# Performance work log

Measured on AMD Instinct MI355X. Metric: run time of the kernel, lower is better.

The kernel has to match this reference:

```python
import jax, jax.numpy as jnp
import numpy as np

N, E = 50000, 600000
NODE_DIM, EDGE_DIM, MSG_DIM = 128, 64, 128


def setup_inputs() -> dict:
    key = jax.random.key(0)
    ks = jax.random.split(key, 8)
    s = 0.05
    return {
        "node_features": jax.random.normal(ks[0], (N, NODE_DIM), jnp.float32),
        "edge_features": jax.random.normal(ks[1], (E, EDGE_DIM), jnp.float32),
        "edge_index": jax.random.randint(ks[2], (2, E), 0, N, jnp.int32),
        "We1": jax.random.normal(ks[3], (2 * NODE_DIM + EDGE_DIM, 32), jnp.float32) * s,
        "be1": jnp.zeros((32,), jnp.float32),
        "We2": jax.random.normal(ks[4], (32, MSG_DIM), jnp.float32) * s,
        "be2": jnp.zeros((MSG_DIM,), jnp.float32),
        "Wn1": jax.random.normal(ks[5], (NODE_DIM + MSG_DIM, 64), jnp.float32) * s,
        "bn1": jnp.zeros((64,), jnp.float32),
        "Wn2": jax.random.normal(ks[6], (64, MSG_DIM), jnp.float32) * s,
        "bn2": jnp.zeros((MSG_DIM,), jnp.float32),
    }


def reference(node_features, edge_features, edge_index,
              We1, be1, We2, be2, Wn1, bn1, Wn2, bn2):
    src, dst = edge_index[0], edge_index[1]
    src_f = node_features[src]            # [E, node_dim] gather
    dst_f = node_features[dst]            # [E, node_dim] gather
    # edge message encoder: 2-layer MLP with ReLU
    edge_in = jnp.concatenate([src_f, dst_f, edge_features], axis=1)  # [E, 2*nd+ed]
    h = jax.nn.relu(edge_in @ We1 + be1)
    edge_msg = jax.nn.relu(h @ We2 + be2)  # [E, msg_dim]
    # node message encoder
    node_in = jnp.concatenate([dst_f, edge_msg], axis=1)  # [E, nd+md]
    h2 = jax.nn.relu(node_in @ Wn1 + bn1)
    node_msg = jax.nn.relu(h2 @ Wn2 + bn2)  # [E, msg_dim]
    # scatter-sum over destination nodes (replaces the O(N) python loop)
    agg = jax.ops.segment_sum(node_msg, dst, num_segments=node_features.shape[0])
    return node_features + agg
```

## Files before the change

### kernel.cpp

```cpp
#include <hip/hip_runtime.h>
#include <hip/hip_bf16.h>

constexpr int N_NODES = 50000;
constexpr int N_EDGES = 600000;
constexpr int ND = 128;
constexpr int ED = 64;
constexpr int MD = 128;
constexpr int H1 = 32;
constexpr int H2 = 64;

typedef __attribute__((ext_vector_type(8))) short short8;
typedef __attribute__((ext_vector_type(4))) float f32x4;
typedef __attribute__((ext_vector_type(4))) unsigned int uint32x4;

#define MFMA16(a, b, c) __builtin_amdgcn_mfma_f32_16x16x32_bf16((a), (b), (c), 0, 0, 0)

constexpr int COUNTS_PAD = 53248;
constexpr size_t WS_MSGS    = 0;
constexpr size_t WS_PRE     = WS_MSGS + (size_t)N_EDGES * MD * 2;
constexpr size_t WS_POS     = WS_PRE + (size_t)N_NODES * 128 * 2;
constexpr size_t WS_COUNTS  = WS_POS + (size_t)N_EDGES * 4;
constexpr size_t WS_OFFSETS = WS_COUNTS + (size_t)COUNTS_PAD * 4;
constexpr size_t WS_WFE     = ((WS_OFFSETS + (size_t)(N_NODES + 1) * 4 + 15) / 16) * 16;
constexpr size_t WS_WFN     = WS_WFE + (size_t)44 * 64 * 16;
constexpr size_t WS_END     = WS_WFN + (size_t)32 * 64 * 16;

__device__ inline float bflo(unsigned u) { return __uint_as_float(u << 16); }
__device__ inline float bfhi(unsigned u) { return __uint_as_float(u & 0xffff0000u); }
__device__ inline short f2bf(float f) {
    __hip_bfloat16 h = __float2bfloat16(f);
    return *reinterpret_cast<short*>(&h);
}
__device__ inline unsigned pkbf(float a, float b) {
    unsigned r;
    asm("v_cvt_pk_bf16_f32 %0, %1, %2" : "=v"(r) : "v"(a), "v"(b));
    return r;
}
__device__ inline unsigned prelu(float a, float b) {
    return pkbf(fmaxf(a, 0.0f), fmaxf(b, 0.0f));
}
__device__ inline short8 pack8(unsigned w0, unsigned w1, unsigned w2, unsigned w3) {
    uint32x4 t{w0, w1, w2, w3};
    return __builtin_bit_cast(short8, t);
}

__device__ inline int hperm(int kt, int kq) {
    return (kt * 2 + ((kq >> 2) & 1)) * 16 + ((kq >> 3) & 3) * 4 + (kq & 3);
}

__global__ __launch_bounds__(256) void wprep(
    const float* __restrict__ We1, const float* __restrict__ We2,
    const float* __restrict__ Wn1, const float* __restrict__ Wn2,
    short8* __restrict__ wfE, short8* __restrict__ wfN)
{
    const int g = blockIdx.x * 256 + threadIdx.x;
    const int lane = g & 63;
    const int f = g >> 6;
    const int m16 = lane & 15, quad = lane >> 4;
    short v[8];
    if (f < 44) {
        #pragma unroll
        for (int j = 0; j < 8; ++j) {
            const int kq = quad * 8 + j;
            float s;
            if (f < 4) {
                const int kt = f >> 1, mt = f & 1;
                s = We1[(size_t)(2 * ND + kt * 32 + kq) * H1 + mt * 16 + m16];
            } else if (f < 12) {
                const int mt = f - 4;
                s = We2[(size_t)hperm(0, kq) * MD + mt * 16 + m16];
            } else if (f < 28) {
                const int ff = f - 12, kt = ff >> 2, mt = ff & 3;
                s = Wn1[(size_t)(ND + hperm(kt, kq)) * H2 + mt * 16 + m16];
            } else {
                const int ff = f - 28, kt = ff >> 3, mt = ff & 7;
                s = Wn2[(size_t)hperm(kt, kq) * MD + mt * 16 + m16];
            }
            v[j] = f2bf(s);
        }
        wfE[g] = short8{v[0], v[1], v[2], v[3], v[4], v[5], v[6], v[7]};
    } else {
        const int ff = f - 44, kt = ff >> 3, nt = ff & 7;
        const int n = nt * 16 + m16;
        #pragma unroll
        for (int j = 0; j < 8; ++j) {
            const int k = kt * 32 + quad * 8 + j;
            float s;
            if (n < 32)      s = We1[(size_t)k * H1 + n];
            else if (n < 64) s = We1[(size_t)(ND + k) * H1 + (n - 32)];
            else             s = Wn1[(size_t)k * H2 + (n - 64)];
            v[j] = f2bf(s);
        }
        wfN[(size_t)(f - 44) * 64 + lane] = short8{v[0], v[1], v[2], v[3], v[4], v[5], v[6], v[7]};
    }
}

__global__ __launch_bounds__(256) void hist_pos(const int* __restrict__ eidx,
                                                int* __restrict__ counts,
                                                int* __restrict__ pos) {
    const int e = blockIdx.x * 256 + threadIdx.x;
    if (e < N_EDGES) pos[e] = atomicAdd(&counts[eidx[N_EDGES + e]], 1);
}

__global__ __launch_bounds__(1024) void scan_kernel(const int* __restrict__ counts,
                                                    int* __restrict__ offsets) {
    constexpr int T = 1024;
    const int tid = threadIdx.x;
    const int base = tid * 52;
    int4 v[13];
    int s = 0;
    const int4* pc = (const int4*)(counts + base);
    #pragma unroll
    for (int i = 0; i < 13; ++i) {
        v[i] = pc[i];
        s += v[i].x + v[i].y + v[i].z + v[i].w;
    }
    __shared__ int sm[T];
    sm[tid] = s;
    __syncthreads();
    for (int off = 1; off < T; off <<= 1) {
        const int t = (tid >= off) ? sm[tid - off] : 0;
        __syncthreads();
        sm[tid] += t;
        __syncthreads();
    }
    int run = sm[tid] - s;
    #pragma unroll
    for (int i = 0; i < 13; ++i) {
        const int idx = base + i * 4;
        if (idx     <= N_NODES) offsets[idx]     = run;  run += v[i].x;
        if (idx + 1 <= N_NODES) offsets[idx + 1] = run;  run += v[i].y;
        if (idx + 2 <= N_NODES) offsets[idx + 2] = run;  run += v[i].z;
        if (idx + 3 <= N_NODES) offsets[idx + 3] = run;  run += v[i].w;
    }
}

__global__ __launch_bounds__(256) void node_pre_mfma(
    const float* __restrict__ nf, const short8* __restrict__ wfN,
    unsigned short* __restrict__ pre)
{
    __shared__ short ost[4][2048];
    const int tid = threadIdx.x;
    const int w = tid >> 6, lane = tid & 63;
    const int m16 = lane & 15, quad = lane >> 4;
    const int n0 = blockIdx.x * 64 + w * 16;

    short8 a[4];
    #pragma unroll
    for (int kt = 0; kt < 4; ++kt) {
        const int node = min(n0 + m16, N_NODES - 1);
        const float* pn = nf + (size_t)node * ND + kt * 32 + quad * 8;
        const float4 f0 = *(const float4*)pn;
        const float4 f1 = *(const float4*)(pn + 4);
        a[kt] = pack8(pkbf(f0.x, f0.y), pkbf(f0.z, f0.w),
                      pkbf(f1.x, f1.y), pkbf(f1.z, f1.w));
    }
    f32x4 acc[8];
    #pragma unroll
    for (int nt = 0; nt < 8; ++nt) acc[nt] = f32x4{0.f, 0.f, 0.f, 0.f};
    #pragma unroll
    for (int kt = 0; kt < 4; ++kt) {
        #pragma unroll
        for (int nt = 0; nt < 8; ++nt)
            acc[nt] = MFMA16(a[kt], wfN[(size_t)(kt * 8 + nt) * 64 + lane], acc[nt]);
    }
    short* o = &ost[w][0];
    #pragma unroll
    for (int nt = 0; nt < 8; ++nt)
        #pragma unroll
        for (int r = 0; r < 4; ++r)
            o[(quad * 4 + r) * 128 + nt * 16 + m16] = f2bf(acc[nt][r]);
    asm volatile("s_waitcnt lgkmcnt(0)" ::: "memory");
    #pragma unroll
    for (int i = 0; i < 4; ++i) {
        const int row = i * 4 + quad;
        const int node = n0 + row;
        if (node < N_NODES) {
            const uint4 v = ((const uint4*)(o + row * 128))[m16];
            *((uint4*)(pre + (size_t)node * 128) + m16) = v;
        }
    }
}

__global__ __launch_bounds__(256, 4) void edge_mfma(
    const float* __restrict__ ef, const int* __restrict__ eidx,
    const unsigned short* __restrict__ pre,
    const int* __restrict__ pos, const int* __restrict__ offsets,
    const short8* __restrict__ wfE,
    const float* __restrict__ be1, const float* __restrict__ be2,
    const float* __restrict__ bn1, const float* __restrict__ bn2,
    unsigned short* __restrict__ msgs)
{
    constexpr int TE = 128;
    __shared__ __align__(16) char sws[4][9216];
    __shared__ int slotlds[TE];

    const int tid = threadIdx.x;
    const int e0 = blockIdx.x * TE;
    const bool hasB = (e0 + 64) < N_EDGES;
    const int w = tid >> 6, lane = tid & 63;
    const int m16 = lane & 15, q = lane >> 4;
    const int er0 = w * 16;
    char* swsb = &sws[w][0];

    float4 efv[2][4];
    {
        const float* pe = ef + (size_t)(e0 + er0 + m16) * ED + q * 8;
        efv[0][0] = *(const float4*)pe;
        efv[0][1] = *(const float4*)(pe + 4);
        efv[0][2] = *(const float4*)(pe + 32);
        efv[0][3] = *(const float4*)(pe + 36);
        if (hasB) {
            const float* pe2 = pe + (size_t)64 * ED;
            efv[1][0] = *(const float4*)pe2;
            efv[1][1] = *(const float4*)(pe2 + 4);
            efv[1][2] = *(const float4*)(pe2 + 32);
            efv[1][3] = *(const float4*)(pe2 + 36);
        }
    }

    {
        const int et = tid >> 2, p4 = tid & 3;
        const int eA = e0 + et;
        const int srcA = eidx[eA];
        const int dstA = eidx[N_EDGES + eA];
        const uint4* paA = (const uint4*)(pre + (size_t)srcA * 128);
        const uint4* pdA = (const uint4*)(pre + (size_t)dstA * 128);
        const uint4 uaA = paA[p4];
        const uint4 udA = pdA[4 + p4];
        const uint4 s0A = pdA[8 + 2 * p4];
        const uint4 s1A = pdA[9 + 2 * p4];
        const int slA = offsets[dstA] + pos[eA];

        uint4 uaB, udB, s0B, s1B;
        int slB = 0;
        if (hasB) {
            const int eB = eA + 64;
            const int srcB = eidx[eB];
            const int dstB = eidx[N_EDGES + eB];
            const uint4* paB = (const uint4*)(pre + (size_t)srcB * 128);
            const uint4* pdB = (const uint4*)(pre + (size_t)dstB * 128);
            uaB = paB[p4];
            udB = pdB[4 + p4];
            s0B = pdB[8 + 2 * p4];
            s1B = pdB[9 + 2 * p4];
            slB = offsets[dstB] + pos[eB];
        }
        const float4 b0 = ((const float4*)be1)[2 * p4];
        const float4 b1 = ((const float4*)be1)[2 * p4 + 1];

        char* wbase = &sws[et >> 4][0] + (et & 15) * 144;
        {
            float4 r0, r1;
            r0.x = bflo(uaA.x) + bflo(udA.x) + b0.x;
            r0.y = bfhi(uaA.x) + bfhi(udA.x) + b0.y;
            r0.z = bflo(uaA.y) + bflo(udA.y) + b0.z;
            r0.w = bfhi(uaA.y) + bfhi(udA.y) + b0.w;
            r1.x = bflo(uaA.z) + bflo(udA.z) + b1.x;
            r1.y = bfhi(uaA.z) + bfhi(udA.z) + b1.y;
            r1.z = bflo(uaA.w) + bflo(udA.w) + b1.z;
            r1.w = bfhi(uaA.w) + bfhi(udA.w) + b1.w;
            *(float4*)(wbase + p4 * 32) = r0;
            *(float4*)(wbase + p4 * 32 + 16) = r1;
            *(uint4*)(wbase + 2304 + p4 * 32) = s0A;
            *(uint4*)(wbase + 2304 + p4 * 32 + 16) = s1A;
            if (p4 == 3) slotlds[et] = slA;
        }
        if (hasB) {
            float4 r0, r1;
            r0.x = bflo(uaB.x) + bflo(udB.x) + b0.x;
            r0.y = bfhi(uaB.x) + bfhi(udB.x) + b0.y;
            r0.z = bflo(uaB.y) + bflo(udB.y) + b0.z;
            r0.w = bfhi(uaB.y) + bfhi(udB.y) + b0.w;
            r1.x = bflo(uaB.z) + bflo(udB.z) + b1.x;
            r1.y = bfhi(uaB.z) + bfhi(udB.z) + b1.y;
            r1.z = bflo(uaB.w) + bflo(udB.w) + b1.z;
            r1.w = bfhi(uaB.w) + bfhi(udB.w) + b1.w;
            *(float4*)(wbase + 4608 + p4 * 32) = r0;
            *(float4*)(wbase + 4608 + p4 * 32 + 16) = r1;
            *(uint4*)(wbase + 4608 + 2304 + p4 * 32) = s0B;
            *(uint4*)(wbase + 4608 + 2304 + p4 * 32 + 16) = s1B;
            if (p4 == 3) slotlds[64 + et] = slB;
        }
    }
    asm volatile("s_waitcnt lgkmcnt(0)" ::: "memory");

    short8 aef[2][2];
    #pragma unroll
    for (int t = 0; t < 2; ++t) {
        aef[t][0] = pack8(pkbf(efv[t][0].x, efv[t][0].y), pkbf(efv[t][0].z, efv[t][0].w),
                          pkbf(efv[t][1].x, efv[t][1].y), pkbf(efv[t][1].z, efv[t][1].w));
        aef[t][1] = pack8(pkbf(efv[t][2].x, efv[t][2].y), pkbf(efv[t][2].z, efv[t][2].w),
                          pkbf(efv[t][3].x, efv[t][3].y), pkbf(efv[t][3].z, efv[t][3].w));
    }

    f32x4 acc1[2][2];
    #pragma unroll
    for (int t = 0; t < 2; ++t)
        #pragma unroll
        for (int mt = 0; mt < 2; ++mt)
            acc1[t][mt] = *(const f32x4*)(swsb + t * 4608 + m16 * 144 + mt * 64 + q * 16);
    #pragma unroll
    for (int kt = 0; kt < 2; ++kt)
        #pragma unroll
        for (int mt = 0; mt < 2; ++mt) {
            const short8 wf = wfE[(size_t)(kt * 2 + mt) * 64 + lane];
            acc1[0][mt] = MFMA16(wf, aef[0][kt], acc1[0][mt]);
            acc1[1][mt] = MFMA16(wf, aef[1][kt], acc1[1][mt]);
        }

    short8 b2[2];
    #pragma unroll
    for (int t = 0; t < 2; ++t)
        b2[t] = pack8(prelu(acc1[t][0][0], acc1[t][0][1]), prelu(acc1[t][0][2], acc1[t][0][3]),
                      prelu(acc1[t][1][0], acc1[t][1][1]), prelu(acc1[t][1][2], acc1[t][1][3]));

    f32x4 acc2[2][8];
    #pragma unroll
    for (int mt = 0; mt < 8; ++mt) {
        const float4 bb = *(const float4*)(be2 + mt * 16 + q * 4);
        const short8 wf = wfE[(size_t)(4 + mt) * 64 + lane];
        acc2[0][mt] = f32x4{bb.x, bb.y, bb.z, bb.w};
        acc2[1][mt] = acc2[0][mt];
        acc2[0][mt] = MFMA16(wf, b2[0], acc2[0][mt]);
        acc2[1][mt] = MFMA16(wf, b2[1], acc2[1][mt]);
    }
    short8 b3[2][4];
    #pragma unroll
    for (int t = 0; t < 2; ++t)
        #pragma unroll
        for (int kt = 0; kt < 4; ++kt)
            b3[t][kt] = pack8(prelu(acc2[t][2 * kt][0], acc2[t][2 * kt][1]),
                              prelu(acc2[t][2 * kt][2], acc2[t][2 * kt][3]),
                              prelu(acc2[t][2 * kt + 1][0], acc2[t][2 * kt + 1][1]),
                              prelu(acc2[t][2 * kt + 1][2], acc2[t][2 * kt + 1][3]));

    f32x4 acc3[2][4];
    #pragma unroll
    for (int mt = 0; mt < 4; ++mt) {
        const float4 bb = *(const float4*)(bn1 + mt * 16 + q * 4);
        #pragma unroll
        for (int t = 0; t < 2; ++t) {
            const uint2 ua = *(const uint2*)(swsb + t * 4608 + 2304 + m16 * 144 + mt * 32 + q * 8);
            acc3[t][mt] = f32x4{bb.x + bflo(ua.x), bb.y + bfhi(ua.x),
                                bb.z + bflo(ua.y), bb.w + bfhi(ua.y)};
        }
    }
    #pragma unroll
    for (int kt = 0; kt < 4; ++kt)
        #pragma unroll
        for (int mt = 0; mt < 4; ++mt) {
            const short8 wf = wfE[(size_t)(12 + kt * 4 + mt) * 64 + lane];
            acc3[0][mt] = MFMA16(wf, b3[0][kt], acc3[0][mt]);
            acc3[1][mt] = MFMA16(wf, b3[1][kt], acc3[1][mt]);
        }
    short8 b4[2][2];
    #pragma unroll
    for (int t = 0; t < 2; ++t)
        #pragma unroll
        for (int kt = 0; kt < 2; ++kt)
            b4[t][kt] = pack8(prelu(acc3[t][2 * kt][0], acc3[t][2 * kt][1]),
                              prelu(acc3[t][2 * kt][2], acc3[t][2 * kt][3]),
                              prelu(acc3[t][2 * kt + 1][0], acc3[t][2 * kt + 1][1]),
                              prelu(acc3[t][2 * kt + 1][2], acc3[t][2 * kt + 1][3]));

    f32x4 acc4[2][8];
    #pragma unroll
    for (int mt = 0; mt < 8; ++mt) {
        const float4 bb = *(const float4*)(bn2 + mt * 16 + q * 4);
        acc4[0][mt] = f32x4{bb.x, bb.y, bb.z, bb.w};
        acc4[1][mt] = acc4[0][mt];
    }
    #pragma unroll
    for (int kt = 0; kt < 2; ++kt)
        #pragma unroll
        for (int mt = 0; mt < 8; ++mt) {
            const short8 wf = wfE[(size_t)(28 + kt * 8 + mt) * 64 + lane];
            acc4[0][mt] = MFMA16(wf, b4[0][kt], acc4[0][mt]);
            acc4[1][mt] = MFMA16(wf, b4[1][kt], acc4[1][mt]);
        }

    #pragma unroll
    for (int t = 0; t < 2; ++t)
        #pragma unroll
        for (int mt = 0; mt < 8; ++mt) {
            uint2 wv;
            wv.x = prelu(acc4[t][mt][0], acc4[t][mt][1]);
            wv.y = prelu(acc4[t][mt][2], acc4[t][mt][3]);
            *(uint2*)(swsb + t * 4608 + m16 * 272 + mt * 32 + q * 8) = wv;
        }
    asm volatile("s_waitcnt lgkmcnt(0)" ::: "memory");

    #pragma unroll
    for (int i = 0; i < 4; ++i) {
        const int row = i * 4 + q;
        const int slA = slotlds[er0 + row];
        const uint4 vA = *(const uint4*)(swsb + row * 272 + m16 * 16);
        *((uint4*)(msgs + (size_t)slA * 128) + m16) = vA;
    }
    if (hasB) {
        #pragma unroll
        for (int i = 0; i < 4; ++i) {
            const int row = i * 4 + q;
            const int slB = slotlds[64 + er0 + row];
            const uint4 vB = *(const uint4*)(swsb + 4608 + row * 272 + m16 * 16);
            *((uint4*)(msgs + (size_t)slB * 128) + m16) = vB;
        }
    }
}

__global__ __launch_bounds__(256) void gather2(
    const float* __restrict__ nf,
    const uint4* __restrict__ msgs4,
    const int* __restrict__ offsets,
    float* __restrict__ out)
{
    const int node = blockIdx.x * 16 + (threadIdx.x >> 4);
    const int m16 = threadIdx.x & 15;

    const float4* pn = (const float4*)(nf + (size_t)node * ND) + m16 * 2;
    const float4 n0 = pn[0];
    const float4 n1 = pn[1];

    const int beg = offsets[node];
    const int end = offsets[node + 1];

    float4 sA0{0.f, 0.f, 0.f, 0.f}, sA1{0.f, 0.f, 0.f, 0.f};
    float4 sB0{0.f, 0.f, 0.f, 0.f}, sB1{0.f, 0.f, 0.f, 0.f};
    const uint4* p = msgs4 + (size_t)beg * 16 + m16;
    int i = beg;
    for (; i + 3 < end; i += 4, p += 64) {
        const uint4 u0 = p[0];
        const uint4 u1 = p[16];
        const uint4 u2 = p[32];
        const uint4 u3 = p[48];
        sA0.x += bflo(u0.x); sA0.y += bfhi(u0.x); sA0.z += bflo(u0.y); sA0.w += bfhi(u0.y);
        sA1.x += bflo(u0.z); sA1.y += bfhi(u0.z); sA1.z += bflo(u0.w); sA1.w += bfhi(u0.w);
        sB0.x += bflo(u1.x); sB0.y += bfhi(u1.x); sB0.z += bflo(u1.y); sB0.w += bfhi(u1.y);
        sB1.x += bflo(u1.z); sB1.y += bfhi(u1.z); sB1.z += bflo(u1.w); sB1.w += bfhi(u1.w);
        sA0.x += bflo(u2.x); sA0.y += bfhi(u2.x); sA0.z += bflo(u2.y); sA0.w += bfhi(u2.y);
        sA1.x += bflo(u2.z); sA1.y += bfhi(u2.z); sA1.z += bflo(u2.w); sA1.w += bfhi(u2.w);
        sB0.x += bflo(u3.x); sB0.y += bfhi(u3.x); sB0.z += bflo(u3.y); sB0.w += bfhi(u3.y);
        sB1.x += bflo(u3.z); sB1.y += bfhi(u3.z); sB1.z += bflo(u3.w); sB1.w += bfhi(u3.w);
    }
    for (; i < end; ++i, p += 16) {
        const uint4 u = p[0];
        sA0.x += bflo(u.x); sA0.y += bfhi(u.x); sA0.z += bflo(u.y); sA0.w += bfhi(u.y);
        sA1.x += bflo(u.z); sA1.y += bfhi(u.z); sA1.z += bflo(u.w); sA1.w += bfhi(u.w);
    }
    float4 s0, s1;
    s0.x = sA0.x + sB0.x + n0.x; s0.y = sA0.y + sB0.y + n0.y;
    s0.z = sA0.z + sB0.z + n0.z; s0.w = sA0.w + sB0.w + n0.w;
    s1.x = sA1.x + sB1.x + n1.x; s1.y = sA1.y + sB1.y + n1.y;
    s1.z = sA1.z + sB1.z + n1.z; s1.w = sA1.w + sB1.w + n1.w;

    float4* po = (float4*)(out + (size_t)node * ND) + m16 * 2;
    po[0] = s0;
    po[1] = s1;
}

extern "C" void kernel_launch(void* const* d_in, const int* in_sizes, int n_in,
                              void* d_out, int out_size, void* d_ws, size_t ws_size,
                              hipStream_t stream) {
    const float* nf  = (const float*)d_in[0];
    const float* ef  = (const float*)d_in[1];
    const int*  eidx = (const int*)d_in[2];
    const float* We1 = (const float*)d_in[3];
    const float* be1 = (const float*)d_in[4];
    const float* We2 = (const float*)d_in[5];
    const float* be2 = (const float*)d_in[6];
    const float* Wn1 = (const float*)d_in[7];
    const float* bn1 = (const float*)d_in[8];
    const float* Wn2 = (const float*)d_in[9];
    const float* bn2 = (const float*)d_in[10];
    float* out = (float*)d_out;

    char* ws = (char*)d_ws;
    unsigned short* msgs = (unsigned short*)(ws + WS_MSGS);
    unsigned short* pre  = (unsigned short*)(ws + WS_PRE);
    int* pos             = (int*)(ws + WS_POS);
    int* counts          = (int*)(ws + WS_COUNTS);
    int* offsets         = (int*)(ws + WS_OFFSETS);
    short8* wfE          = (short8*)(ws + WS_WFE);
    short8* wfN          = (short8*)(ws + WS_WFN);
    (void)ws_size; (void)WS_END;

    hipMemsetAsync(counts, 0, (size_t)COUNTS_PAD * 4, stream);
    wprep<<<19, 256, 0, stream>>>(We1, We2, Wn1, Wn2, wfE, wfN);
    hist_pos<<<(N_EDGES + 255) / 256, 256, 0, stream>>>(eidx, counts, pos);
    scan_kernel<<<1, 1024, 0, stream>>>(counts, offsets);
    node_pre_mfma<<<(N_NODES + 63) / 64, 256, 0, stream>>>(nf, wfN, pre);
    edge_mfma<<<(N_EDGES + 127) / 128, 256, 0, stream>>>(
        ef, eidx, pre, pos, offsets, wfE, be1, be2, bn1, bn2, msgs);
    gather2<<<N_NODES / 16, 256, 0, stream>>>(nf, (const uint4*)msgs, offsets, out);
}
```

Before: 422.6 us.

## Make edge MLP kernel persistent with atomic work queue and LDS-resident weights

Turns the edge MLP kernel into a persistent kernel of 768 blocks. Each wavefront grabs 32-edge work units from an atomic counter, placed in the zeroed counts buffer. Weights and biases are loaded into LDS once per block instead of being re-read from global memory per tile. Gathered node data is loaded straight into MFMA register fragments and messages are written directly to global memory, with no LDS staging. This trades less staging traffic and lower per-block setup for one atomic per unit, and scattered uint2 stores that may coalesce less well.

```diff
diff --git a/kernel.cpp b/kernel.cpp
--- a/kernel.cpp
+++ b/kernel.cpp
@@ -16,6 +16,7 @@
 #define MFMA16(a, b, c) __builtin_amdgcn_mfma_f32_16x16x32_bf16((a), (b), (c), 0, 0, 0)
 
 constexpr int COUNTS_PAD = 53248;
+constexpr int WCTR_IDX   = 51200;
 constexpr size_t WS_MSGS    = 0;
 constexpr size_t WS_PRE     = WS_MSGS + (size_t)N_EDGES * MD * 2;
 constexpr size_t WS_POS     = WS_PRE + (size_t)N_NODES * 128 * 2;
@@ -182,229 +183,189 @@
     }
 }
 
-__global__ __launch_bounds__(256, 4) void edge_mfma(
+__global__ __launch_bounds__(256, 3) void edge_mfma(
     const float* __restrict__ ef, const int* __restrict__ eidx,
     const unsigned short* __restrict__ pre,
     const int* __restrict__ pos, const int* __restrict__ offsets,
     const short8* __restrict__ wfE,
     const float* __restrict__ be1, const float* __restrict__ be2,
     const float* __restrict__ bn1, const float* __restrict__ bn2,
+    int* __restrict__ wctr,
     unsigned short* __restrict__ msgs)
 {
-    constexpr int TE = 128;
-    __shared__ __align__(16) char sws[4][9216];
-    __shared__ int slotlds[TE];
+    constexpr int NUNITS = N_EDGES / 32;
+    __shared__ short8 wlds[44 * 64];
+    __shared__ float blds[352];
 
     const int tid = threadIdx.x;
-    const int e0 = blockIdx.x * TE;
-    const bool hasB = (e0 + 64) < N_EDGES;
-    const int w = tid >> 6, lane = tid & 63;
+    for (int i = tid; i < 44 * 64; i += 256) wlds[i] = wfE[i];
+    for (int i = tid; i < 352; i += 256) {
+        float v;
+        if (i < 32)       v = be1[i];
+        else if (i < 160) v = be2[i - 32];
+        else if (i < 224) v = bn1[i - 160];
+        else              v = bn2[i - 224];
+        blds[i] = v;
+    }
+    __syncthreads();
+
+    const int lane = tid & 63;
     const int m16 = lane & 15, q = lane >> 4;
-    const int er0 = w * 16;
-    char* swsb = &sws[w][0];
-
-    float4 efv[2][4];
-    {
-        const float* pe = ef + (size_t)(e0 + er0 + m16) * ED + q * 8;
-        efv[0][0] = *(const float4*)pe;
-        efv[0][1] = *(const float4*)(pe + 4);
-        efv[0][2] = *(const float4*)(pe + 32);
-        efv[0][3] = *(const float4*)(pe + 36);
-        if (hasB) {
-            const float* pe2 = pe + (size_t)64 * ED;
-            efv[1][0] = *(const float4*)pe2;
-            efv[1][1] = *(const float4*)(pe2 + 4);
-            efv[1][2] = *(const float4*)(pe2 + 32);
-            efv[1][3] = *(const float4*)(pe2 + 36);
-        }
-    }
-
-    {
-        const int et = tid >> 2, p4 = tid & 3;
-        const int eA = e0 + et;
-        const int srcA = eidx[eA];
-        const int dstA = eidx[N_EDGES + eA];
-        const uint4* paA = (const uint4*)(pre + (size_t)srcA * 128);
-        const uint4* pdA = (const uint4*)(pre + (size_t)dstA * 128);
-        const uint4 uaA = paA[p4];
-        const uint4 udA = pdA[4 + p4];
-        const uint4 s0A = pdA[8 + 2 * p4];
-        const uint4 s1A = pdA[9 + 2 * p4];
-        const int slA = offsets[dstA] + pos[eA];
-
-        uint4 uaB, udB, s0B, s1B;
-        int slB = 0;
-        if (hasB) {
-            const int eB = eA + 64;
-            const int srcB = eidx[eB];
-            const int dstB = eidx[N_EDGES + eB];
-            const uint4* paB = (const uint4*)(pre + (size_t)srcB * 128);
-            const uint4* pdB = (const uint4*)(pre + (size_t)dstB * 128);
-            uaB = paB[p4];
-            udB = pdB[4 + p4];
-            s0B = pdB[8 + 2 * p4];
-            s1B = pdB[9 + 2 * p4];
-            slB = offsets[dstB] + pos[eB];
-        }
-        const float4 b0 = ((const float4*)be1)[2 * p4];
-        const float4 b1 = ((const float4*)be1)[2 * p4 + 1];
-
-        char* wbase = &sws[et >> 4][0] + (et & 15) * 144;
+
+    while (true) {
+        int u = 0;
+        if (lane == 0) u = atomicAdd(wctr, 1);
+        u = __shfl(u, 0);
+        if (u >= NUNITS) break;
+
+        const int eA = u * 32 + m16;
+        const int eB = eA + 16;
+
+        int src[2], dst[2], slot[2];
+        src[0] = eidx[eA];            dst[0] = eidx[N_EDGES + eA];
+        src[1] = eidx[eB];            dst[1] = eidx[N_EDGES + eB];
+        slot[0] = offsets[dst[0]] + pos[eA];
+        slot[1] = offsets[dst[1]] + pos[eB];
+
+        uint2 a1[2][2], a2[2][2], a3[2][4];
+        #pragma unroll
+        for (int t = 0; t < 2; ++t) {
+            const char* ps = (const char*)pre + (size_t)src[t] * 256 + q * 8;
+            const char* pd = (const char*)pre + (size_t)dst[t] * 256 + q * 8;
+            a1[t][0] = *(const uint2*)(ps);
+            a1[t][1] = *(const uint2*)(ps + 32);
+            a2[t][0] = *(const uint2*)(pd + 64);
+            a2[t][1] = *(const uint2*)(pd + 96);
+            a3[t][0] = *(const uint2*)(pd + 128);
+            a3[t][1] = *(const uint2*)(pd + 160);
+            a3[t][2] = *(const uint2*)(pd + 192);
+            a3[t][3] = *(const uint2*)(pd + 224);
+        }
+
+        float4 efv[2][4];
         {
-            float4 r0, r1;
-            r0.x = bflo(uaA.x) + bflo(udA.x) + b0.x;
-            r0.y = bfhi(uaA.x) + bfhi(udA.x) + b0.y;
-            r0.z = bflo(uaA.y) + bflo(udA.y) + b0.z;
-            r0.w = bfhi(uaA.y) + bfhi(udA.y) + b0.w;
-            r1.x = bflo(uaA.z) + bflo(udA.z) + b1.x;
-            r1.y = bfhi(uaA.z) + bfhi(udA.z) + b1.y;
-            r1.z = bflo(uaA.w) + bflo(udA.w) + b1.z;
-            r1.w = bfhi(uaA.w) + bfhi(udA.w) + b1.w;
-            *(float4*)(wbase + p4 * 32) = r0;
-            *(float4*)(wbase + p4 * 32 + 16) = r1;
-            *(uint4*)(wbase + 2304 + p4 * 32) = s0A;
-            *(uint4*)(wbase + 2304 + p4 * 32 + 16) = s1A;
-            if (p4 == 3) slotlds[et] = slA;
-        }
-        if (hasB) {
-            float4 r0, r1;
-            r0.x = bflo(uaB.x) + bflo(udB.x) + b0.x;
-            r0.y = bfhi(uaB.x) + bfhi(udB.x) + b0.y;
-            r0.z = bflo(uaB.y) + bflo(udB.y) + b0.z;
-            r0.w = bfhi(uaB.y) + bfhi(udB.y) + b0.w;
-            r1.x = bflo(uaB.z) + bflo(udB.z) + b1.x;
-            r1.y = bfhi(uaB.z) + bfhi(udB.z) + b1.y;
-            r1.z = bflo(uaB.w) + bflo(udB.w) + b1.z;
-            r1.w = bfhi(uaB.w) + bfhi(udB.w) + b1.w;
-            *(float4*)(wbase + 4608 + p4 * 32) = r0;
-            *(float4*)(wbase + 4608 + p4 * 32 + 16) = r1;
-            *(uint4*)(wbase + 4608 + 2304 + p4 * 32) = s0B;
-            *(uint4*)(wbase + 4608 + 2304 + p4 * 32 + 16) = s1B;
-            if (p4 == 3) slotlds[64 + et] = slB;
-        }
-    }
-    asm volatile("s_waitcnt lgkmcnt(0)" ::: "memory");
-
-    short8 aef[2][2];
-    #pragma unroll
-    for (int t = 0; t < 2; ++t) {
-        aef[t][0] = pack8(pkbf(efv[t][0].x, efv[t][0].y), pkbf(efv[t][0].z, efv[t][0].w),
-                          pkbf(efv[t][1].x, efv[t][1].y), pkbf(efv[t][1].z, efv[t][1].w));
-        aef[t][1] = pack8(pkbf(efv[t][2].x, efv[t][2].y), pkbf(efv[t][2].z, efv[t][2].w),
-                          pkbf(efv[t][3].x, efv[t][3].y), pkbf(efv[t][3].z, efv[t][3].w));
-    }
-
-    f32x4 acc1[2][2];
-    #pragma unroll
-    for (int t = 0; t < 2; ++t)
-        #pragma unroll
-        for (int mt = 0; mt < 2; ++mt)
-            acc1[t][mt] = *(const f32x4*)(swsb + t * 4608 + m16 * 144 + mt * 64 + q * 16);
-    #pragma unroll
-    for (int kt = 0; kt < 2; ++kt)
+            const float* peA = ef + (size_t)eA * ED + q * 8;
+            efv[0][0] = *(const float4*)peA;
+            efv[0][1] = *(const float4*)(peA + 4);
+            efv[0][2] = *(const float4*)(peA + 32);
+            efv[0][3] = *(const float4*)(peA + 36);
+            const float* peB = ef + (size_t)eB * ED + q * 8;
+            efv[1][0] = *(const float4*)peB;
+            efv[1][1] = *(const float4*)(peB + 4);
+            efv[1][2] = *(const float4*)(peB + 32);
+            efv[1][3] = *(const float4*)(peB + 36);
+        }
+        short8 aef[2][2];
+        #pragma unroll
+        for (int t = 0; t < 2; ++t) {
+            aef[t][0] = pack8(pkbf(efv[t][0].x, efv[t][0].y), pkbf(efv[t][0].z, efv[t][0].w),
+                              pkbf(efv[t][1].x, efv[t][1].y), pkbf(efv[t][1].z, efv[t][1].w));
+            aef[t][1] = pack8(pkbf(efv[t][2].x, efv[t][2].y), pkbf(efv[t][2].z, efv[t][2].w),
+                              pkbf(efv[t][3].x, efv[t][3].y), pkbf(efv[t][3].z, efv[t][3].w));
+        }
+
+        f32x4 acc1[2][2];
         #pragma unroll
         for (int mt = 0; mt < 2; ++mt) {
-            const short8 wf = wfE[(size_t)(kt * 2 + mt) * 64 + lane];
-            acc1[0][mt] = MFMA16(wf, aef[0][kt], acc1[0][mt]);
-            acc1[1][mt] = MFMA16(wf, aef[1][kt], acc1[1][mt]);
-        }
-
-    short8 b2[2];
-    #pragma unroll
-    for (int t = 0; t < 2; ++t)
-        b2[t] = pack8(prelu(acc1[t][0][0], acc1[t][0][1]), prelu(acc1[t][0][2], acc1[t][0][3]),
-                      prelu(acc1[t][1][0], acc1[t][1][1]), prelu(acc1[t][1][2], acc1[t][1][3]));
-
-    f32x4 acc2[2][8];
-    #pragma unroll
-    for (int mt = 0; mt < 8; ++mt) {
-        const float4 bb = *(const float4*)(be2 + mt * 16 + q * 4);
-        const short8 wf = wfE[(size_t)(4 + mt) * 64 + lane];
-        acc2[0][mt] = f32x4{bb.x, bb.y, bb.z, bb.w};
-        acc2[1][mt] = acc2[0][mt];
-        acc2[0][mt] = MFMA16(wf, b2[0], acc2[0][mt]);
-        acc2[1][mt] = MFMA16(wf, b2[1], acc2[1][mt]);
-    }
-    short8 b3[2][4];
-    #pragma unroll
-    for (int t = 0; t < 2; ++t)
+            const float4 bb = *(const float4*)&blds[mt * 16 + q * 4];
+            #pragma unroll
+            for (int t = 0; t < 2; ++t) {
+                acc1[t][mt][0] = bflo(a1[t][mt].x) + bflo(a2[t][mt].x) + bb.x;
+                acc1[t][mt][1] = bfhi(a1[t][mt].x) + bfhi(a2[t][mt].x) + bb.y;
+                acc1[t][mt][2] = bflo(a1[t][mt].y) + bflo(a2[t][mt].y) + bb.z;
+                acc1[t][mt][3] = bfhi(a1[t][mt].y) + bfhi(a2[t][mt].y) + bb.w;
+            }
+        }
+        #pragma unroll
+        for (int kt = 0; kt < 2; ++kt)
+            #pragma unroll
+            for (int mt = 0; mt < 2; ++mt) {
+                const short8 wf = wlds[(kt * 2 + mt) * 64 + lane];
+                acc1[0][mt] = MFMA16(wf, aef[0][kt], acc1[0][mt]);
+                acc1[1][mt] = MFMA16(wf, aef[1][kt], acc1[1][mt]);
+            }
+        short8 b2[2];
+        #pragma unroll
+        for (int t = 0; t < 2; ++t)
+            b2[t] = pack8(prelu(acc1[t][0][0], acc1[t][0][1]), prelu(acc1[t][0][2], acc1[t][0][3]),
+                          prelu(acc1[t][1][0], acc1[t][1][1]), prelu(acc1[t][1][2], acc1[t][1][3]));
+
+        f32x4 acc2[2][8];
+        #pragma unroll
+        for (int mt = 0; mt < 8; ++mt) {
+            const float4 bb = *(const float4*)&blds[32 + mt * 16 + q * 4];
+            const short8 wf = wlds[(4 + mt) * 64 + lane];
+            acc2[0][mt] = f32x4{bb.x, bb.y, bb.z, bb.w};
+            acc2[1][mt] = acc2[0][mt];
+            acc2[0][mt] = MFMA16(wf, b2[0], acc2[0][mt]);
+            acc2[1][mt] = MFMA16(wf, b2[1], acc2[1][mt]);
+        }
+        short8 b3[2][4];
+        #pragma unroll
+        for (int t = 0; t < 2; ++t)
+            #pragma unroll
+            for (int kt = 0; kt < 4; ++kt)
+                b3[t][kt] = pack8(prelu(acc2[t][2 * kt][0], acc2[t][2 * kt][1]),
+                                  prelu(acc2[t][2 * kt][2], acc2[t][2 * kt][3]),
+                                  prelu(acc2[t][2 * kt + 1][0], acc2[t][2 * kt + 1][1]),
+                                  prelu(acc2[t][2 * kt + 1][2], acc2[t][2 * kt + 1][3]));
+
+        f32x4 acc3[2][4];
+        #pragma unroll
+        for (int mt = 0; mt < 4; ++mt) {
+            const float4 bb = *(const float4*)&blds[160 + mt * 16 + q * 4];
+            #pragma unroll
+            for (int t = 0; t < 2; ++t) {
+                acc3[t][mt][0] = bb.x + bflo(a3[t][mt].x);
+                acc3[t][mt][1] = bb.y + bfhi(a3[t][mt].x);
+                acc3[t][mt][2] = bb.z + bflo(a3[t][mt].y);
+                acc3[t][mt][3] = bb.w + bfhi(a3[t][mt].y);
+            }
+        }
         #pragma unroll
         for (int kt = 0; kt < 4; ++kt)
-            b3[t][kt] = pack8(prelu(acc2[t][2 * kt][0], acc2[t][2 * kt][1]),
-                              prelu(acc2[t][2 * kt][2], acc2[t][2 * kt][3]),
-                              prelu(acc2[t][2 * kt + 1][0], acc2[t][2 * kt + 1][1]),
-                              prelu(acc2[t][2 * kt + 1][2], acc2[t][2 * kt + 1][3]));
-
-    f32x4 acc3[2][4];
-    #pragma unroll
-    for (int mt = 0; mt < 4; ++mt) {
-        const float4 bb = *(const float4*)(bn1 + mt * 16 + q * 4);
+            #pragma unroll
+            for (int mt = 0; mt < 4; ++mt) {
+                const short8 wf = wlds[(12 + kt * 4 + mt) * 64 + lane];
+                acc3[0][mt] = MFMA16(wf, b3[0][kt], acc3[0][mt]);
+                acc3[1][mt] = MFMA16(wf, b3[1][kt], acc3[1][mt]);
+            }
+        short8 b4[2][2];
+        #pragma unroll
+        for (int t = 0; t < 2; ++t)
+            #pragma unroll
+            for (int kt = 0; kt < 2; ++kt)
+                b4[t][kt] = pack8(prelu(acc3[t][2 * kt][0], acc3[t][2 * kt][1]),
+                                  prelu(acc3[t][2 * kt][2], acc3[t][2 * kt][3]),
+                                  prelu(acc3[t][2 * kt + 1][0], acc3[t][2 * kt + 1][1]),
+                                  prelu(acc3[t][2 * kt + 1][2], acc3[t][2 * kt + 1][3]));
+
+        f32x4 acc4[2][8];
+        #pragma unroll
+        for (int mt = 0; mt < 8; ++mt) {
+            const float4 bb = *(const float4*)&blds[224 + mt * 16 + q * 4];
+            acc4[0][mt] = f32x4{bb.x, bb.y, bb.z, bb.w};
+            acc4[1][mt] = acc4[0][mt];
+        }
+        #pragma unroll
+        for (int kt = 0; kt < 2; ++kt)
+            #pragma unroll
+            for (int mt = 0; mt < 8; ++mt) {
+                const short8 wf = wlds[(28 + kt * 8 + mt) * 64 + lane];
+                acc4[0][mt] = MFMA16(wf, b4[0][kt], acc4[0][mt]);
+                acc4[1][mt] = MFMA16(wf, b4[1][kt], acc4[1][mt]);
+            }
+
         #pragma unroll
         for (int t = 0; t < 2; ++t) {
-            const uint2 ua = *(const uint2*)(swsb + t * 4608 + 2304 + m16 * 144 + mt * 32 + q * 8);
-            acc3[t][mt] = f32x4{bb.x + bflo(ua.x), bb.y + bfhi(ua.x),
-                                bb.z + bflo(ua.y), bb.w + bfhi(ua.y)};
-        }
-    }
-    #pragma unroll
-    for (int kt = 0; kt < 4; ++kt)
-        #pragma unroll
-        for (int mt = 0; mt < 4; ++mt) {
-            const short8 wf = wfE[(size_t)(12 + kt * 4 + mt) * 64 + lane];
-            acc3[0][mt] = MFMA16(wf, b3[0][kt], acc3[0][mt]);
-            acc3[1][mt] = MFMA16(wf, b3[1][kt], acc3[1][mt]);
-        }
-    short8 b4[2][2];
-    #pragma unroll
-    for (int t = 0; t < 2; ++t)
-        #pragma unroll
-        for (int kt = 0; kt < 2; ++kt)
-            b4[t][kt] = pack8(prelu(acc3[t][2 * kt][0], acc3[t][2 * kt][1]),
-                              prelu(acc3[t][2 * kt][2], acc3[t][2 * kt][3]),
-                              prelu(acc3[t][2 * kt + 1][0], acc3[t][2 * kt + 1][1]),
-                              prelu(acc3[t][2 * kt + 1][2], acc3[t][2 * kt + 1][3]));
-
-    f32x4 acc4[2][8];
-    #pragma unroll
-    for (int mt = 0; mt < 8; ++mt) {
-        const float4 bb = *(const float4*)(bn2 + mt * 16 + q * 4);
-        acc4[0][mt] = f32x4{bb.x, bb.y, bb.z, bb.w};
-        acc4[1][mt] = acc4[0][mt];
-    }
-    #pragma unroll
-    for (int kt = 0; kt < 2; ++kt)
-        #pragma unroll
-        for (int mt = 0; mt < 8; ++mt) {
-            const short8 wf = wfE[(size_t)(28 + kt * 8 + mt) * 64 + lane];
-            acc4[0][mt] = MFMA16(wf, b4[0][kt], acc4[0][mt]);
-            acc4[1][mt] = MFMA16(wf, b4[1][kt], acc4[1][mt]);
-        }
-
-    #pragma unroll
-    for (int t = 0; t < 2; ++t)
-        #pragma unroll
-        for (int mt = 0; mt < 8; ++mt) {
-            uint2 wv;
-            wv.x = prelu(acc4[t][mt][0], acc4[t][mt][1]);
-            wv.y = prelu(acc4[t][mt][2], acc4[t][mt][3]);
-            *(uint2*)(swsb + t * 4608 + m16 * 272 + mt * 32 + q * 8) = wv;
-        }
-    asm volatile("s_waitcnt lgkmcnt(0)" ::: "memory");
-
-    #pragma unroll
-    for (int i = 0; i < 4; ++i) {
-        const int row = i * 4 + q;
-        const int slA = slotlds[er0 + row];
-        const uint4 vA = *(const uint4*)(swsb + row * 272 + m16 * 16);
-        *((uint4*)(msgs + (size_t)slA * 128) + m16) = vA;
-    }
-    if (hasB) {
-        #pragma unroll
-        for (int i = 0; i < 4; ++i) {
-            const int row = i * 4 + q;
-            const int slB = slotlds[64 + er0 + row];
-            const uint4 vB = *(const uint4*)(swsb + 4608 + row * 272 + m16 * 16);
-            *((uint4*)(msgs + (size_t)slB * 128) + m16) = vB;
+            char* pm = (char*)msgs + (size_t)slot[t] * 256 + q * 8;
+            #pragma unroll
+            for (int mt = 0; mt < 8; ++mt) {
+                uint2 wv;
+                wv.x = prelu(acc4[t][mt][0], acc4[t][mt][1]);
+                wv.y = prelu(acc4[t][mt][2], acc4[t][mt][3]);
+                *(uint2*)(pm + mt * 32) = wv;
+            }
         }
     }
 }
@@ -483,6 +444,7 @@
     int* offsets         = (int*)(ws + WS_OFFSETS);
     short8* wfE          = (short8*)(ws + WS_WFE);
     short8* wfN          = (short8*)(ws + WS_WFN);
+    int* wctr            = counts + WCTR_IDX;
     (void)ws_size; (void)WS_END;
 
     hipMemsetAsync(counts, 0, (size_t)COUNTS_PAD * 4, stream);
@@ -490,7 +452,7 @@
     hist_pos<<<(N_EDGES + 255) / 256, 256, 0, stream>>>(eidx, counts, pos);
     scan_kernel<<<1, 1024, 0, stream>>>(counts, offsets);
     node_pre_mfma<<<(N_NODES + 63) / 64, 256, 0, stream>>>(nf, wfN, pre);
-    edge_mfma<<<(N_EDGES + 127) / 128, 256, 0, stream>>>(
-        ef, eidx, pre, pos, offsets, wfE, be1, be2, bn1, bn2, msgs);
+    edge_mfma<<<768, 256, 0, stream>>>(
+        ef, eidx, pre, pos, offsets, wfE, be1, be2, bn1, bn2, wctr, msgs);
     gather2<<<N_NODES / 16, 256, 0, stream>>>(nf, (const uint4*)msgs, offsets, out);
 }
```

Result: slower. 571.7 us (+35.3%).

## Replace sort-based segment sum with direct float atomic scatter into output

Applied to the files above, without the earlier changes.

Drops the histogram, scan, bf16 message buffer and gather kernel. The node_pre kernel now copies node features into the output, and the edge kernel atomically adds each ReLU'd fp32 message straight into out[dst]. This removes three launches, the count memset and the round trip of a 150MB bf16 message buffer. In exchange it issues 77M scalar float atomics, which may contend on high-degree nodes and makes the summation order nondeterministic.

```diff
diff --git a/kernel.cpp b/kernel.cpp
--- a/kernel.cpp
+++ b/kernel.cpp
@@ -95,55 +95,24 @@
     }
 }
 
-__global__ __launch_bounds__(256) void hist_pos(const int* __restrict__ eidx,
-                                                int* __restrict__ counts,
-                                                int* __restrict__ pos) {
-    const int e = blockIdx.x * 256 + threadIdx.x;
-    if (e < N_EDGES) pos[e] = atomicAdd(&counts[eidx[N_EDGES + e]], 1);
-}
-
-__global__ __launch_bounds__(1024) void scan_kernel(const int* __restrict__ counts,
-                                                    int* __restrict__ offsets) {
-    constexpr int T = 1024;
-    const int tid = threadIdx.x;
-    const int base = tid * 52;
-    int4 v[13];
-    int s = 0;
-    const int4* pc = (const int4*)(counts + base);
-    #pragma unroll
-    for (int i = 0; i < 13; ++i) {
-        v[i] = pc[i];
-        s += v[i].x + v[i].y + v[i].z + v[i].w;
-    }
-    __shared__ int sm[T];
-    sm[tid] = s;
-    __syncthreads();
-    for (int off = 1; off < T; off <<= 1) {
-        const int t = (tid >= off) ? sm[tid - off] : 0;
-        __syncthreads();
-        sm[tid] += t;
-        __syncthreads();
-    }
-    int run = sm[tid] - s;
-    #pragma unroll
-    for (int i = 0; i < 13; ++i) {
-        const int idx = base + i * 4;
-        if (idx     <= N_NODES) offsets[idx]     = run;  run += v[i].x;
-        if (idx + 1 <= N_NODES) offsets[idx + 1] = run;  run += v[i].y;
-        if (idx + 2 <= N_NODES) offsets[idx + 2] = run;  run += v[i].z;
-        if (idx + 3 <= N_NODES) offsets[idx + 3] = run;  run += v[i].w;
-    }
-}
-
 __global__ __launch_bounds__(256) void node_pre_mfma(
     const float* __restrict__ nf, const short8* __restrict__ wfN,
-    unsigned short* __restrict__ pre)
+    unsigned short* __restrict__ pre, float* __restrict__ out)
 {
     __shared__ short ost[4][2048];
     const int tid = threadIdx.x;
     const int w = tid >> 6, lane = tid & 63;
     const int m16 = lane & 15, quad = lane >> 4;
     const int n0 = blockIdx.x * 64 + w * 16;
+
+    {
+        const int nbase = blockIdx.x * 64;
+        const int nrem = min(64, N_NODES - nbase);
+        const float4* s4 = (const float4*)(nf + (size_t)nbase * ND);
+        float4* d4 = (float4*)(out + (size_t)nbase * ND);
+        const int tot = nrem * (ND / 4);
+        for (int i = tid; i < tot; i += 256) d4[i] = s4[i];
+    }
 
     short8 a[4];
     #pragma unroll
@@ -185,15 +154,13 @@
 __global__ __launch_bounds__(256, 4) void edge_mfma(
     const float* __restrict__ ef, const int* __restrict__ eidx,
     const unsigned short* __restrict__ pre,
-    const int* __restrict__ pos, const int* __restrict__ offsets,
     const short8* __restrict__ wfE,
     const float* __restrict__ be1, const float* __restrict__ be2,
     const float* __restrict__ bn1, const float* __restrict__ bn2,
-    unsigned short* __restrict__ msgs)
+    float* __restrict__ out)
 {
     constexpr int TE = 128;
     __shared__ __align__(16) char sws[4][9216];
-    __shared__ int slotlds[TE];
 
     const int tid = threadIdx.x;
     const int e0 = blockIdx.x * TE;
@@ -230,10 +197,8 @@
         const uint4 udA = pdA[4 + p4];
         const uint4 s0A = pdA[8 + 2 * p4];
         const uint4 s1A = pdA[9 + 2 * p4];
-        const int slA = offsets[dstA] + pos[eA];
 
         uint4 uaB, udB, s0B, s1B;
-        int slB = 0;
         if (hasB) {
             const int eB = eA + 64;
             const int srcB = eidx[eB];
@@ -244,7 +209,6 @@
             udB = pdB[4 + p4];
             s0B = pdB[8 + 2 * p4];
             s1B = pdB[9 + 2 * p4];
-            slB = offsets[dstB] + pos[eB];
         }
         const float4 b0 = ((const float4*)be1)[2 * p4];
         const float4 b1 = ((const float4*)be1)[2 * p4 + 1];
@@ -264,7 +228,6 @@
             *(float4*)(wbase + p4 * 32 + 16) = r1;
             *(uint4*)(wbase + 2304 + p4 * 32) = s0A;
             *(uint4*)(wbase + 2304 + p4 * 32 + 16) = s1A;
-            if (p4 == 3) slotlds[et] = slA;
         }
         if (hasB) {
             float4 r0, r1;
@@ -280,7 +243,6 @@
             *(float4*)(wbase + 4608 + p4 * 32 + 16) = r1;
             *(uint4*)(wbase + 4608 + 2304 + p4 * 32) = s0B;
             *(uint4*)(wbase + 4608 + 2304 + p4 * 32 + 16) = s1B;
-            if (p4 == 3) slotlds[64 + et] = slB;
         }
     }
     asm volatile("s_waitcnt lgkmcnt(0)" ::: "memory");
@@ -381,82 +343,18 @@
         }
 
     #pragma unroll
-    for (int t = 0; t < 2; ++t)
-        #pragma unroll
-        for (int mt = 0; mt < 8; ++mt) {
-            uint2 wv;
-            wv.x = prelu(acc4[t][mt][0], acc4[t][mt][1]);
-            wv.y = prelu(acc4[t][mt][2], acc4[t][mt][3]);
-            *(uint2*)(swsb + t * 4608 + m16 * 272 + mt * 32 + q * 8) = wv;
-        }
-    asm volatile("s_waitcnt lgkmcnt(0)" ::: "memory");
-
-    #pragma unroll
-    for (int i = 0; i < 4; ++i) {
-        const int row = i * 4 + q;
-        const int slA = slotlds[er0 + row];
-        const uint4 vA = *(const uint4*)(swsb + row * 272 + m16 * 16);
-        *((uint4*)(msgs + (size_t)slA * 128) + m16) = vA;
-    }
-    if (hasB) {
-        #pragma unroll
-        for (int i = 0; i < 4; ++i) {
-            const int row = i * 4 + q;
-            const int slB = slotlds[64 + er0 + row];
-            const uint4 vB = *(const uint4*)(swsb + 4608 + row * 272 + m16 * 16);
-            *((uint4*)(msgs + (size_t)slB * 128) + m16) = vB;
-        }
-    }
-}
-
-__global__ __launch_bounds__(256) void gather2(
-    const float* __restrict__ nf,
-    const uint4* __restrict__ msgs4,
-    const int* __restrict__ offsets,
-    float* __restrict__ out)
-{
-    const int node = blockIdx.x * 16 + (threadIdx.x >> 4);
-    const int m16 = threadIdx.x & 15;
-
-    const float4* pn = (const float4*)(nf + (size_t)node * ND) + m16 * 2;
-    const float4 n0 = pn[0];
-    const float4 n1 = pn[1];
-
-    const int beg = offsets[node];
-    const int end = offsets[node + 1];
-
-    float4 sA0{0.f, 0.f, 0.f, 0.f}, sA1{0.f, 0.f, 0.f, 0.f};
-    float4 sB0{0.f, 0.f, 0.f, 0.f}, sB1{0.f, 0.f, 0.f, 0.f};
-    const uint4* p = msgs4 + (size_t)beg * 16 + m16;
-    int i = beg;
-    for (; i + 3 < end; i += 4, p += 64) {
-        const uint4 u0 = p[0];
-        const uint4 u1 = p[16];
-        const uint4 u2 = p[32];
-        const uint4 u3 = p[48];
-        sA0.x += bflo(u0.x); sA0.y += bfhi(u0.x); sA0.z += bflo(u0.y); sA0.w += bfhi(u0.y);
-        sA1.x += bflo(u0.z); sA1.y += bfhi(u0.z); sA1.z += bflo(u0.w); sA1.w += bfhi(u0.w);
-        sB0.x += bflo(u1.x); sB0.y += bfhi(u1.x); sB0.z += bflo(u1.y); sB0.w += bfhi(u1.y);
-        sB1.x += bflo(u1.z); sB1.y += bfhi(u1.z); sB1.z += bflo(u1.w); sB1.w += bfhi(u1.w);
-        sA0.x += bflo(u2.x); sA0.y += bfhi(u2.x); sA0.z += bflo(u2.y); sA0.w += bfhi(u2.y);
-        sA1.x += bflo(u2.z); sA1.y += bfhi(u2.z); sA1.z += bflo(u2.w); sA1.w += bfhi(u2.w);
-        sB0.x += bflo(u3.x); sB0.y += bfhi(u3.x); sB0.z += bflo(u3.y); sB0.w += bfhi(u3.y);
-        sB1.x += bflo(u3.z); sB1.y += bfhi(u3.z); sB1.z += bflo(u3.w); sB1.w += bfhi(u3.w);
-    }
-    for (; i < end; ++i, p += 16) {
-        const uint4 u = p[0];
-        sA0.x += bflo(u.x); sA0.y += bfhi(u.x); sA0.z += bflo(u.y); sA0.w += bfhi(u.y);
-        sA1.x += bflo(u.z); sA1.y += bfhi(u.z); sA1.z += bflo(u.w); sA1.w += bfhi(u.w);
-    }
-    float4 s0, s1;
-    s0.x = sA0.x + sB0.x + n0.x; s0.y = sA0.y + sB0.y + n0.y;
-    s0.z = sA0.z + sB0.z + n0.z; s0.w = sA0.w + sB0.w + n0.w;
-    s1.x = sA1.x + sB1.x + n1.x; s1.y = sA1.y + sB1.y + n1.y;
-    s1.z = sA1.z + sB1.z + n1.z; s1.w = sA1.w + sB1.w + n1.w;
-
-    float4* po = (float4*)(out + (size_t)node * ND) + m16 * 2;
-    po[0] = s0;
-    po[1] = s1;
+    for (int t = 0; t < 2; ++t) {
+        if (t == 0 || hasB) {
+            const int dstv = eidx[N_EDGES + e0 + t * 64 + er0 + m16];
+            float* po = out + (size_t)dstv * ND + q * 4;
+            #pragma unroll
+            for (int mt = 0; mt < 8; ++mt) {
+                #pragma unroll
+                for (int r = 0; r < 4; ++r)
+                    atomicAdd(po + mt * 16 + r, fmaxf(acc4[t][mt][r], 0.0f));
+            }
+        }
+    }
 }
 
 extern "C" void kernel_launch(void* const* d_in, const int* in_sizes, int n_in,
@@ -476,21 +374,13 @@
     float* out = (float*)d_out;
 
     char* ws = (char*)d_ws;
-    unsigned short* msgs = (unsigned short*)(ws + WS_MSGS);
     unsigned short* pre  = (unsigned short*)(ws + WS_PRE);
-    int* pos             = (int*)(ws + WS_POS);
-    int* counts          = (int*)(ws + WS_COUNTS);
-    int* offsets         = (int*)(ws + WS_OFFSETS);
     short8* wfE          = (short8*)(ws + WS_WFE);
     short8* wfN          = (short8*)(ws + WS_WFN);
     (void)ws_size; (void)WS_END;
 
-    hipMemsetAsync(counts, 0, (size_t)COUNTS_PAD * 4, stream);
     wprep<<<19, 256, 0, stream>>>(We1, We2, Wn1, Wn2, wfE, wfN);
-    hist_pos<<<(N_EDGES + 255) / 256, 256, 0, stream>>>(eidx, counts, pos);
-    scan_kernel<<<1, 1024, 0, stream>>>(counts, offsets);
-    node_pre_mfma<<<(N_NODES + 63) / 64, 256, 0, stream>>>(nf, wfN, pre);
+    node_pre_mfma<<<(N_NODES + 63) / 64, 256, 0, stream>>>(nf, wfN, pre, out);
     edge_mfma<<<(N_EDGES + 127) / 128, 256, 0, stream>>>(
-        ef, eidx, pre, pos, offsets, wfE, be1, be2, bn1, bn2, msgs);
-    gather2<<<N_NODES / 16, 256, 0, stream>>>(nf, (const uint4*)msgs, offsets, out);
-}
+        ef, eidx, pre, wfE, be1, be2, bn1, bn2, out);
+}
```

Result: slower. 1.235 ms (+192.3%).
